# Optimization experiments

Hardware: AMD Instinct MI355X
Metric: run time of the kernel (lower is better)

The kernel has to match this reference:

```python
import jax, jax.numpy as jnp
import numpy as np

POS_KL_W = 0.1
NEG_KL_W = 0.02
ORDER_W = 0.5
N_BINS = 1000
SIGMA = 0.1
EPS = 1e-09


def setup_inputs() -> dict:
    key = jax.random.key(0)
    k1, k2, k3 = jax.random.split(key, 3)
    N, D, C = 256, 512, 16
    T_F = jax.random.normal(k1, (N, D), dtype=jnp.float32)
    S_F = jax.random.normal(k2, (N, D), dtype=jnp.float32)
    labels = jax.random.uniform(k3, (N, C), dtype=jnp.float32)  # argmax -> class ids
    return {"T_F": T_F, "S_F": S_F, "labels": labels}


def _histograms_and_means(x, pos_labels, neg_labels, t):
    # x: [N, D]; L2-normalize rows (eps matches F.normalize default 1e-12)
    norm = jnp.maximum(jnp.linalg.norm(x, axis=-1, keepdims=True), 1e-12)
    xn = x / norm
    cos = xn @ xn.T                      # [N, N]
    dists = cos.reshape(-1)              # [N*N]
    # Gaussian soft-binning: [N*N, N_BINS] (the big memory-bound intermediate)
    delta = jnp.exp(-0.5 * ((dists[:, None] - t[None, :]) / SIGMA) ** 2)
    neg_w = neg_labels.reshape(-1)
    pos_w = pos_labels.reshape(-1)
    neg_p = (neg_w @ delta) / jnp.sum(neg_w)   # [N_BINS]
    pos_p = (pos_w @ delta) / jnp.sum(pos_w)   # [N_BINS]
    E_pos = jnp.sum(cos * pos_labels, axis=-1) / jnp.sum(pos_labels, axis=-1)  # [N]
    E_neg = jnp.sum(cos * neg_labels, axis=-1) / jnp.sum(neg_labels, axis=-1)  # [N]
    return neg_p, pos_p, E_neg, E_pos


def _kl(anchor, dist):
    # torch F.kl_div(log(dist+eps), anchor+eps, reduction='batchmean'); batch dim is 1
    a = anchor + EPS
    d = dist + EPS
    return jnp.sum(a * (jnp.log(a) - jnp.log(d)))


def reference(T_F, S_F, labels):
    N = T_F.shape[0]
    t = jnp.arange(-1.0, 1.0, 2.0 / N_BINS, dtype=jnp.float32)  # [1000] bin centers
    lab = jnp.argmax(labels, axis=-1)                            # [N]
    grid = (lab[None, :] == lab[:, None]).astype(jnp.float32)    # [N, N]
    neg_labels = 1.0 - grid
    pos_labels = grid * (1.0 - jnp.eye(N, dtype=jnp.float32))

    neg_t, pos_t, E_neg_t, E_pos_t = _histograms_and_means(T_F, pos_labels, neg_labels, t)
    neg_s, pos_s, E_neg_s, E_pos_s = _histograms_and_means(S_F, pos_labels, neg_labels, t)

    pos_kl = POS_KL_W * _kl(pos_t, pos_s)
    neg_kl = NEG_KL_W * _kl(neg_t, neg_s)
    o1 = jnp.mean(jnp.abs(E_pos_t - E_pos_s))
    o2 = jnp.mean(jnp.abs(E_neg_t - E_neg_s))
    o3 = jnp.mean(E_pos_s - E_neg_s)
    order_loss = ORDER_W * (o1 + o2 + o3)
    return pos_kl + neg_kl + order_loss
```

## Files before the change

kernel.cpp:

```cpp
#include <hip/hip_runtime.h>
#include <math.h>

#define N 256
#define D 512
#define C 16
#define NBINS 1000
#define MCELL 1000
#define MSTRIDE 1024
#define EPSF 1e-9f
#define KEXP2 -72.134752f
#define TAILB 64

__device__ inline float waveReduceSum(float v) {
#pragma unroll
    for (int off = 32; off > 0; off >>= 1) v += __shfl_down(v, off, 64);
    return v;
}
__device__ inline double waveReduceSumD(double v) {
#pragma unroll
    for (int off = 32; off > 0; off >>= 1) v += __shfl_down(v, off, 64);
    return v;
}

__global__ void k_prep(const float* __restrict__ T, const float* __restrict__ S,
                       const float* __restrict__ labels,
                       float* __restrict__ xn, float* __restrict__ xnT,
                       int* __restrict__ lab, float* __restrict__ mg,
                       unsigned int* __restrict__ cnt) {
    int i = blockIdx.x;
    int mat = blockIdx.y;
    int tid = threadIdx.x;
    int bid = mat * 256 + i;
    if (bid < 48) mg[bid * 256 + tid] = 0.f;
    if (bid == 48 && tid == 0) cnt[0] = 0u;
    const float* in = mat ? S : T;
    if (mat == 0 && tid == 0) {
        float best = labels[i * C];
        int bi = 0;
#pragma unroll
        for (int c = 1; c < C; ++c) {
            float v = labels[i * C + c];
            if (v > best) { best = v; bi = c; }
        }
        lab[i] = bi;
    }
    float v0 = in[i * D + tid];
    float v1 = in[i * D + 256 + tid];
    float ss = v0 * v0 + v1 * v1;
    ss = waveReduceSum(ss);
    __shared__ float lds[4];
    __shared__ float inv_s;
    int wid = tid >> 6, lane = tid & 63;
    if (lane == 0) lds[wid] = ss;
    __syncthreads();
    if (tid == 0) {
        float tot = lds[0] + lds[1] + lds[2] + lds[3];
        inv_s = 1.0f / fmaxf(sqrtf(tot), 1e-12f);
    }
    __syncthreads();
    float inv = inv_s;
    float* xnm = xn + mat * (N * D);
    float* xnTm = xnT + mat * (N * D);
    float a = v0 * inv, b = v1 * inv;
    xnm[i * D + tid] = a;
    xnm[i * D + 256 + tid] = b;
    xnTm[tid * N + i] = a;
    xnTm[(tid + 256) * N + i] = b;
}

__global__ void __launch_bounds__(256) k_main(
        const float* __restrict__ xn, const float* __restrict__ xnT,
        const int* __restrict__ lab, float* __restrict__ mg,
        float* __restrict__ Earr, float* __restrict__ cpos) {
    int mat = blockIdx.y;
    int i0 = blockIdx.x * 4;
    int j = threadIdx.x;
    const float* xnm = xn + mat * (N * D);
    const float* xc = xnT + mat * (N * D);
    __shared__ float rows[D][4];
    __shared__ float mom[6 * 1024];
    for (int i = j; i < 6 * 1024; i += 256) mom[i] = 0.f;
#pragma unroll
    for (int r = 0; r < 4; ++r) {
        rows[j][r] = xnm[(i0 + r) * D + j];
        rows[j + 256][r] = xnm[(i0 + r) * D + 256 + j];
    }
    int labj = lab[j];
    int li0 = lab[i0], li1 = lab[i0 + 1], li2 = lab[i0 + 2], li3 = lab[i0 + 3];
    __syncthreads();

    float a0 = 0.f, a1 = 0.f, a2 = 0.f, a3 = 0.f;
#pragma unroll 8
    for (int k = 0; k < D; ++k) {
        float xb = xc[k * N + j];
        float4 rr = *(const float4*)&rows[k][0];
        a0 = fmaf(rr.x, xb, a0);
        a1 = fmaf(rr.y, xb, a1);
        a2 = fmaf(rr.z, xb, a2);
        a3 = fmaf(rr.w, xb, a3);
    }
    float av[4] = {a0, a1, a2, a3};
    int liv[4] = {li0, li1, li2, li3};
    float wp[4], vA[4];
#pragma unroll
    for (int r = 0; r < 4; ++r) {
        bool diag = (j == i0 + r);
        wp[r] = (labj == liv[r] && !diag) ? 1.f : 0.f;
        vA[r] = diag ? 0.f : av[r];
        if (!diag) {
            float d = av[r];
            int jc = (int)floorf((d + 1.f) * 500.f);
            jc = max(0, min(jc, MCELL - 1));
            float del = d - (-1.f + ((float)jc + 0.5f) * 0.002f);
            float dd = del * del;
            atomicAdd(&mom[jc], 1.f);
            atomicAdd(&mom[MSTRIDE + jc], del);
            atomicAdd(&mom[2 * MSTRIDE + jc], dd);
            if (wp[r] > 0.f) {
                atomicAdd(&mom[3 * MSTRIDE + jc], 1.f);
                atomicAdd(&mom[4 * MSTRIDE + jc], del);
                atomicAdd(&mom[5 * MSTRIDE + jc], dd);
            }
        }
    }

    float r0 = waveReduceSum(vA[0]);
    float r1 = waveReduceSum(av[0] * wp[0]);
    float r2 = waveReduceSum(wp[0]);
    float r3 = waveReduceSum(vA[1]);
    float r4 = waveReduceSum(av[1] * wp[1]);
    float r5 = waveReduceSum(wp[1]);
    float r6 = waveReduceSum(vA[2]);
    float r7 = waveReduceSum(av[2] * wp[2]);
    float r8 = waveReduceSum(wp[2]);
    float r9 = waveReduceSum(vA[3]);
    float r10 = waveReduceSum(av[3] * wp[3]);
    float r11 = waveReduceSum(wp[3]);
    __shared__ float red[4][12];
    int wid = j >> 6, lane = j & 63;
    if (lane == 0) {
        red[wid][0] = r0;  red[wid][1] = r1;  red[wid][2] = r2;
        red[wid][3] = r3;  red[wid][4] = r4;  red[wid][5] = r5;
        red[wid][6] = r6;  red[wid][7] = r7;  red[wid][8] = r8;
        red[wid][9] = r9;  red[wid][10] = r10; red[wid][11] = r11;
    }
    __syncthreads();

    for (int i = j; i < 6 * 1024; i += 256) {
        float v = mom[i];
        if (v != 0.f) atomicAdd(&mg[mat * 6144 + i], v);
    }
    if (j < 4) {
        float sA = 0, sP = 0, cP = 0;
        for (int w = 0; w < 4; ++w) {
            sA += red[w][j * 3 + 0];
            sP += red[w][j * 3 + 1];
            cP += red[w][j * 3 + 2];
        }
        int row = i0 + j;
        Earr[(mat * 2 + 0) * N + row] = sP / cP;
        Earr[(mat * 2 + 1) * N + row] = (sA - sP) / (255.f - cP);
        if (mat == 0) cpos[row] = cP;
    }
}

__global__ void __launch_bounds__(256) k_tail(const float* __restrict__ mg,
                                              const float* __restrict__ Earr,
                                              const float* __restrict__ cpos,
                                              float* __restrict__ pkl,
                                              unsigned int* __restrict__ cnt,
                                              float* __restrict__ out) {
    int b = blockIdx.x;
    int tid = threadIdx.x;
    int wid = tid >> 6, lane = tid & 63;
    __shared__ float sm[12288];
    __shared__ float binres[16][4];
    __shared__ float kterm[16][2];
    __shared__ float credL[4];
    __shared__ unsigned int old_s;
    __shared__ double dred[4][5];

    for (int i = tid; i < 3072; i += 256)
        ((float4*)sm)[i] = ((const float4*)mg)[i];

    float cv = cpos[tid];
    cv = waveReduceSum(cv);
    if (lane == 0) credL[wid] = cv;
    __syncthreads();
    float pcnt = credL[0] + credL[1] + credL[2] + credL[3];
    float ncnt = 65280.f - pcnt;

    int u = tid >> 4, sub = tid & 15;
    int bin = b * 16 + u;
    float t = -1.f + 0.002f * (float)bin;
    float paT = 0.f, saT = 0.f, paS = 0.f, saS = 0.f;
    for (int c = sub; c < MCELL; c += 16) {
        float m0T = sm[c], m0S = sm[6144 + c];
        if (m0T == 0.f && m0S == 0.f) continue;
        float cj = -1.f + ((float)c + 0.5f) * 0.002f;
        float q = cj - t;
        float q2 = q * q;
        if (q2 < 0.5f) {
            float E = __builtin_amdgcn_exp2f(KEXP2 * q2);
            float u1 = 100.f * q;
            float w2 = fmaf(0.5f * u1, u1, -50.f);
            saT = fmaf(E, fmaf(w2, sm[2048 + c], fmaf(-u1, sm[1024 + c], m0T)), saT);
            paT = fmaf(E, fmaf(w2, sm[5120 + c], fmaf(-u1, sm[4096 + c], sm[3072 + c])), paT);
            saS = fmaf(E, fmaf(w2, sm[6144 + 2048 + c], fmaf(-u1, sm[6144 + 1024 + c], m0S)), saS);
            paS = fmaf(E, fmaf(w2, sm[6144 + 5120 + c], fmaf(-u1, sm[6144 + 4096 + c], sm[6144 + 3072 + c])), paS);
        }
    }
#pragma unroll
    for (int off = 1; off < 16; off <<= 1) {
        paT += __shfl_xor(paT, off, 16);
        saT += __shfl_xor(saT, off, 16);
        paS += __shfl_xor(paS, off, 16);
        saS += __shfl_xor(saS, off, 16);
    }
    if (sub == 0) {
        binres[u][0] = paT; binres[u][1] = saT;
        binres[u][2] = paS; binres[u][3] = saS;
    }
    __syncthreads();

    if (tid < 16) {
        int bn = b * 16 + tid;
        float pk = 0.f, nk = 0.f;
        if (bn < NBINS) {
            float hpT = binres[tid][0], hsT = binres[tid][1];
            float hpS = binres[tid][2], hsS = binres[tid][3];
            float pt = hpT / pcnt;
            float nt = (hsT - hpT) / ncnt;
            float ps = hpS / pcnt;
            float ns = (hsS - hpS) / ncnt;
            pk = (pt + EPSF) * (__logf(pt + EPSF) - __logf(ps + EPSF));
            nk = (nt + EPSF) * (__logf(nt + EPSF) - __logf(ns + EPSF));
        }
        kterm[tid][0] = pk;
        kterm[tid][1] = nk;
    }
    __syncthreads();
    if (tid == 0) {
        float a = 0.f, bb = 0.f;
        for (int q = 0; q < 16; ++q) { a += kterm[q][0]; bb += kterm[q][1]; }
        pkl[b * 2] = a;
        pkl[b * 2 + 1] = bb;
        __threadfence();
        old_s = atomicAdd(cnt, 1u);
    }
    __syncthreads();
    if (old_s != TAILB - 1) return;

    __threadfence();
    double a = 0.0, bb = 0.0;
    if (tid < TAILB) {
        volatile const float* vp = pkl;
        a = (double)vp[2 * tid];
        bb = (double)vp[2 * tid + 1];
    }
    a = waveReduceSumD(a);
    bb = waveReduceSumD(bb);
    double o1, o2, o3;
    {
        float ept = Earr[0 * N + tid];
        float ent = Earr[1 * N + tid];
        float eps_ = Earr[2 * N + tid];
        float ens = Earr[3 * N + tid];
        o1 = fabs((double)ept - (double)eps_);
        o2 = fabs((double)ent - (double)ens);
        o3 = (double)eps_ - (double)ens;
    }
    o1 = waveReduceSumD(o1);
    o2 = waveReduceSumD(o2);
    o3 = waveReduceSumD(o3);
    if (lane == 0) {
        dred[wid][0] = a;  dred[wid][1] = bb;
        dred[wid][2] = o1; dred[wid][3] = o2; dred[wid][4] = o3;
    }
    __syncthreads();
    if (tid == 0) {
        double A = dred[0][0], B = dred[0][1];
        double Co = 0, Do = 0, Eo = 0;
        for (int w = 0; w < 4; ++w) {
            Co += dred[w][2]; Do += dred[w][3]; Eo += dred[w][4];
        }
        double loss = 0.1 * A + 0.02 * B + 0.5 * ((Co + Do + Eo) / (double)N);
        out[0] = (float)loss;
    }
}

extern "C" void kernel_launch(void* const* d_in, const int* in_sizes, int n_in,
                              void* d_out, int out_size, void* d_ws, size_t ws_size,
                              hipStream_t stream) {
    const float* T = (const float*)d_in[0];
    const float* S = (const float*)d_in[1];
    const float* labels = (const float*)d_in[2];
    float* out = (float*)d_out;

    float* ws = (float*)d_ws;
    float* xn = ws;
    float* xnT = xn + 2 * N * D;
    float* mg = xnT + 2 * N * D;
    float* Earr = mg + 12288;
    float* cpos = Earr + 1024;
    float* pkl = cpos + 256;
    unsigned int* cnt = (unsigned int*)(pkl + 128);
    int* lab = (int*)(cnt + 1);

    k_prep<<<dim3(N, 2), 256, 0, stream>>>(T, S, labels, xn, xnT, lab, mg, cnt);
    k_main<<<dim3(N / 4, 2), 256, 0, stream>>>(xn, xnT, lab, mg, Earr, cpos);
    k_tail<<<TAILB, 256, 0, stream>>>(mg, Earr, cpos, pkl, cnt, out);
}
```

Measured before the change: 52.56 us.

## Fuse row normalization into Gram kernel and drop normalized/transposed copies

The prep kernel no longer normalizes or transposes the inputs. It now only zeroes the accumulators and computes the label argmax, using 13 blocks instead of 512. The main kernel reads raw rows directly, recomputing each row's squared norm inside the dot-product loop and scaling the dot products by both inverse norms afterwards. Blocks now handle 2 rows instead of 4, which doubles the grid but means each block re-reads the full 512 KB matrix with uncoalesced per-thread row strides and does more duplicate norm work and global atomic flushes of the moment histogram.

```diff
diff --git a/kernel.cpp b/kernel.cpp
--- a/kernel.cpp
+++ b/kernel.cpp
@@ -22,135 +22,112 @@
     return v;
 }
 
-__global__ void k_prep(const float* __restrict__ T, const float* __restrict__ S,
-                       const float* __restrict__ labels,
-                       float* __restrict__ xn, float* __restrict__ xnT,
-                       int* __restrict__ lab, float* __restrict__ mg,
-                       unsigned int* __restrict__ cnt) {
-    int i = blockIdx.x;
-    int mat = blockIdx.y;
+__global__ void k_prep(const float* __restrict__ labels, int* __restrict__ lab,
+                       float* __restrict__ mg, unsigned int* __restrict__ cnt) {
+    int b = blockIdx.x;
     int tid = threadIdx.x;
-    int bid = mat * 256 + i;
-    if (bid < 48) mg[bid * 256 + tid] = 0.f;
-    if (bid == 48 && tid == 0) cnt[0] = 0u;
-    const float* in = mat ? S : T;
-    if (mat == 0 && tid == 0) {
-        float best = labels[i * C];
+    if (b < 12) {
+        ((float4*)mg)[b * 256 + tid] = make_float4(0.f, 0.f, 0.f, 0.f);
+    } else {
+        if (tid == 0) cnt[0] = 0u;
+        float best = labels[tid * C];
         int bi = 0;
 #pragma unroll
         for (int c = 1; c < C; ++c) {
-            float v = labels[i * C + c];
+            float v = labels[tid * C + c];
             if (v > best) { best = v; bi = c; }
         }
-        lab[i] = bi;
-    }
-    float v0 = in[i * D + tid];
-    float v1 = in[i * D + 256 + tid];
-    float ss = v0 * v0 + v1 * v1;
-    ss = waveReduceSum(ss);
-    __shared__ float lds[4];
-    __shared__ float inv_s;
-    int wid = tid >> 6, lane = tid & 63;
-    if (lane == 0) lds[wid] = ss;
-    __syncthreads();
-    if (tid == 0) {
-        float tot = lds[0] + lds[1] + lds[2] + lds[3];
-        inv_s = 1.0f / fmaxf(sqrtf(tot), 1e-12f);
-    }
-    __syncthreads();
-    float inv = inv_s;
-    float* xnm = xn + mat * (N * D);
-    float* xnTm = xnT + mat * (N * D);
-    float a = v0 * inv, b = v1 * inv;
-    xnm[i * D + tid] = a;
-    xnm[i * D + 256 + tid] = b;
-    xnTm[tid * N + i] = a;
-    xnTm[(tid + 256) * N + i] = b;
+        lab[tid] = bi;
+    }
 }
 
 __global__ void __launch_bounds__(256) k_main(
-        const float* __restrict__ xn, const float* __restrict__ xnT,
+        const float* __restrict__ T, const float* __restrict__ S,
         const int* __restrict__ lab, float* __restrict__ mg,
         float* __restrict__ Earr, float* __restrict__ cpos) {
     int mat = blockIdx.y;
-    int i0 = blockIdx.x * 4;
+    int i0 = blockIdx.x * 2;
     int j = threadIdx.x;
-    const float* xnm = xn + mat * (N * D);
-    const float* xc = xnT + mat * (N * D);
-    __shared__ float rows[D][4];
-    __shared__ float mom[6 * 1024];
-    for (int i = j; i < 6 * 1024; i += 256) mom[i] = 0.f;
-#pragma unroll
-    for (int r = 0; r < 4; ++r) {
-        rows[j][r] = xnm[(i0 + r) * D + j];
-        rows[j + 256][r] = xnm[(i0 + r) * D + 256 + j];
-    }
+    const float* X = mat ? S : T;
+    __shared__ float rowA[D], rowB[D];
+    __shared__ float invs[256];
+    __shared__ float mom[6 * MSTRIDE];
+    __shared__ float red[4][6];
+    for (int i = j; i < 6 * MSTRIDE; i += 256) mom[i] = 0.f;
+    rowA[j] = X[i0 * D + j];
+    rowA[j + 256] = X[i0 * D + 256 + j];
+    rowB[j] = X[(i0 + 1) * D + j];
+    rowB[j + 256] = X[(i0 + 1) * D + 256 + j];
+    __syncthreads();
+
+    float d0 = 0.f, d1 = 0.f, ssq = 0.f;
+    {
+        const float4* xrow = (const float4*)(X + (size_t)j * D);
+        const float4* rA4 = (const float4*)rowA;
+        const float4* rB4 = (const float4*)rowB;
+#pragma unroll 16
+        for (int k4 = 0; k4 < 128; ++k4) {
+            float4 xj = xrow[k4];
+            float4 a4 = rA4[k4];
+            float4 b4 = rB4[k4];
+            d0 = fmaf(a4.x, xj.x, fmaf(a4.y, xj.y, fmaf(a4.z, xj.z, fmaf(a4.w, xj.w, d0))));
+            d1 = fmaf(b4.x, xj.x, fmaf(b4.y, xj.y, fmaf(b4.z, xj.z, fmaf(b4.w, xj.w, d1))));
+            ssq = fmaf(xj.x, xj.x, fmaf(xj.y, xj.y, fmaf(xj.z, xj.z, fmaf(xj.w, xj.w, ssq))));
+        }
+    }
+    invs[j] = 1.0f / fmaxf(sqrtf(ssq), 1e-12f);
+    __syncthreads();
+    float invj = invs[j];
+    float av0 = d0 * invs[i0] * invj;
+    float av1 = d1 * invs[i0 + 1] * invj;
+
     int labj = lab[j];
-    int li0 = lab[i0], li1 = lab[i0 + 1], li2 = lab[i0 + 2], li3 = lab[i0 + 3];
-    __syncthreads();
-
-    float a0 = 0.f, a1 = 0.f, a2 = 0.f, a3 = 0.f;
-#pragma unroll 8
-    for (int k = 0; k < D; ++k) {
-        float xb = xc[k * N + j];
-        float4 rr = *(const float4*)&rows[k][0];
-        a0 = fmaf(rr.x, xb, a0);
-        a1 = fmaf(rr.y, xb, a1);
-        a2 = fmaf(rr.z, xb, a2);
-        a3 = fmaf(rr.w, xb, a3);
-    }
-    float av[4] = {a0, a1, a2, a3};
-    int liv[4] = {li0, li1, li2, li3};
-    float wp[4], vA[4];
-#pragma unroll
-    for (int r = 0; r < 4; ++r) {
-        bool diag = (j == i0 + r);
-        wp[r] = (labj == liv[r] && !diag) ? 1.f : 0.f;
-        vA[r] = diag ? 0.f : av[r];
-        if (!diag) {
-            float d = av[r];
-            int jc = (int)floorf((d + 1.f) * 500.f);
-            jc = max(0, min(jc, MCELL - 1));
-            float del = d - (-1.f + ((float)jc + 0.5f) * 0.002f);
-            float dd = del * del;
-            atomicAdd(&mom[jc], 1.f);
-            atomicAdd(&mom[MSTRIDE + jc], del);
-            atomicAdd(&mom[2 * MSTRIDE + jc], dd);
-            if (wp[r] > 0.f) {
-                atomicAdd(&mom[3 * MSTRIDE + jc], 1.f);
-                atomicAdd(&mom[4 * MSTRIDE + jc], del);
-                atomicAdd(&mom[5 * MSTRIDE + jc], dd);
-            }
-        }
-    }
-
-    float r0 = waveReduceSum(vA[0]);
-    float r1 = waveReduceSum(av[0] * wp[0]);
-    float r2 = waveReduceSum(wp[0]);
-    float r3 = waveReduceSum(vA[1]);
-    float r4 = waveReduceSum(av[1] * wp[1]);
-    float r5 = waveReduceSum(wp[1]);
-    float r6 = waveReduceSum(vA[2]);
-    float r7 = waveReduceSum(av[2] * wp[2]);
-    float r8 = waveReduceSum(wp[2]);
-    float r9 = waveReduceSum(vA[3]);
-    float r10 = waveReduceSum(av[3] * wp[3]);
-    float r11 = waveReduceSum(wp[3]);
-    __shared__ float red[4][12];
+    bool diag0 = (j == i0), diag1 = (j == i0 + 1);
+    float wp0 = (labj == lab[i0] && !diag0) ? 1.f : 0.f;
+    float wp1 = (labj == lab[i0 + 1] && !diag1) ? 1.f : 0.f;
+
+    if (!diag0) {
+        int jc = (int)floorf((av0 + 1.f) * 500.f);
+        jc = max(0, min(jc, MCELL - 1));
+        float del = av0 - (-1.f + ((float)jc + 0.5f) * 0.002f);
+        float dd = del * del;
+        atomicAdd(&mom[jc], 1.f);
+        atomicAdd(&mom[MSTRIDE + jc], del);
+        atomicAdd(&mom[2 * MSTRIDE + jc], dd);
+        if (wp0 > 0.f) {
+            atomicAdd(&mom[3 * MSTRIDE + jc], 1.f);
+            atomicAdd(&mom[4 * MSTRIDE + jc], del);
+            atomicAdd(&mom[5 * MSTRIDE + jc], dd);
+        }
+    }
+    if (!diag1) {
+        int jc = (int)floorf((av1 + 1.f) * 500.f);
+        jc = max(0, min(jc, MCELL - 1));
+        float del = av1 - (-1.f + ((float)jc + 0.5f) * 0.002f);
+        float dd = del * del;
+        atomicAdd(&mom[jc], 1.f);
+        atomicAdd(&mom[MSTRIDE + jc], del);
+        atomicAdd(&mom[2 * MSTRIDE + jc], dd);
+        if (wp1 > 0.f) {
+            atomicAdd(&mom[3 * MSTRIDE + jc], 1.f);
+            atomicAdd(&mom[4 * MSTRIDE + jc], del);
+            atomicAdd(&mom[5 * MSTRIDE + jc], dd);
+        }
+    }
+
+    float r0 = waveReduceSum(diag0 ? 0.f : av0);
+    float r1 = waveReduceSum(av0 * wp0);
+    float r2 = waveReduceSum(wp0);
+    float r3 = waveReduceSum(diag1 ? 0.f : av1);
+    float r4 = waveReduceSum(av1 * wp1);
+    float r5 = waveReduceSum(wp1);
     int wid = j >> 6, lane = j & 63;
     if (lane == 0) {
-        red[wid][0] = r0;  red[wid][1] = r1;  red[wid][2] = r2;
-        red[wid][3] = r3;  red[wid][4] = r4;  red[wid][5] = r5;
-        red[wid][6] = r6;  red[wid][7] = r7;  red[wid][8] = r8;
-        red[wid][9] = r9;  red[wid][10] = r10; red[wid][11] = r11;
-    }
-    __syncthreads();
-
-    for (int i = j; i < 6 * 1024; i += 256) {
-        float v = mom[i];
-        if (v != 0.f) atomicAdd(&mg[mat * 6144 + i], v);
-    }
-    if (j < 4) {
+        red[wid][0] = r0; red[wid][1] = r1; red[wid][2] = r2;
+        red[wid][3] = r3; red[wid][4] = r4; red[wid][5] = r5;
+    }
+    __syncthreads();
+    if (j < 2) {
         float sA = 0, sP = 0, cP = 0;
         for (int w = 0; w < 4; ++w) {
             sA += red[w][j * 3 + 0];
@@ -161,6 +138,10 @@
         Earr[(mat * 2 + 0) * N + row] = sP / cP;
         Earr[(mat * 2 + 1) * N + row] = (sA - sP) / (255.f - cP);
         if (mat == 0) cpos[row] = cP;
+    }
+    for (int i = j; i < 6 * MSTRIDE; i += 256) {
+        float v = mom[i];
+        if (v != 0.f) atomicAdd(&mg[mat * 6144 + i], v);
     }
 }
 
@@ -298,16 +279,14 @@
     float* out = (float*)d_out;
 
     float* ws = (float*)d_ws;
-    float* xn = ws;
-    float* xnT = xn + 2 * N * D;
-    float* mg = xnT + 2 * N * D;
+    float* mg = ws;
     float* Earr = mg + 12288;
     float* cpos = Earr + 1024;
     float* pkl = cpos + 256;
     unsigned int* cnt = (unsigned int*)(pkl + 128);
     int* lab = (int*)(cnt + 1);
 
-    k_prep<<<dim3(N, 2), 256, 0, stream>>>(T, S, labels, xn, xnT, lab, mg, cnt);
-    k_main<<<dim3(N / 4, 2), 256, 0, stream>>>(xn, xnT, lab, mg, Earr, cpos);
+    k_prep<<<13, 256, 0, stream>>>(labels, lab, mg, cnt);
+    k_main<<<dim3(N / 2, 2), 256, 0, stream>>>(T, S, lab, mg, Earr, cpos);
     k_tail<<<TAILB, 256, 0, stream>>>(mg, Earr, cpos, pkl, cnt, out);
 }
```

New measurement: 48.22 us. 1.09x faster.
